# Optimization experiments

Hardware: AMD Instinct MI355X
Metric: run time of the kernel (lower is better)

The kernel has to match this reference:

```python
import jax, jax.numpy as jnp
import numpy as np

N_NODES = 100000

def setup_inputs() -> dict:
    key = jax.random.key(0)
    k1, k2, k3 = jax.random.split(key, 3)
    x = jax.random.normal(k1, (N_NODES, 64), dtype=jnp.float32)
    edge_index = jax.random.randint(k2, (2, 1600000), 0, N_NODES, dtype=jnp.int64)
    edge_weights = jax.random.uniform(k3, (1600000,), dtype=jnp.float32)
    weight = jnp.ones((1,), dtype=jnp.float32)  # MyConv.weight, reset to 1
    return {"x": x, "edge_index": edge_index, "edge_weights": edge_weights, "weight": weight}

def reference(x, edge_index, edge_weights, weight):
    src = edge_index[0]  # x_j (source nodes, messages flow source->target)
    dst = edge_index[1]  # aggregation target i
    # message: edge_weight * x_j ; aggregate: scatter-add at dst
    msgs = edge_weights[:, None] * x[src]              # [E, D]
    agg = jax.ops.segment_sum(msgs, dst, num_segments=N_NODES)  # [N, D]
    # conv1: x + weight * aggregate, then relu (Encoder only applies conv1)
    return jax.nn.relu(x + weight * agg)
```

## Files before the change

kernel.cpp:

```cpp
#include <hip/hip_runtime.h>

constexpr int N_NODES = 100000;
constexpr int D       = 64;
constexpr int N_EDGES = 1600000;
constexpr int OUT_N4  = N_NODES * D / 4;

constexpr int NPB   = 128;
constexpr int NBUCK = (N_NODES + NPB - 1) / NPB;
constexpr int BCAP  = 2560;
constexpr int CPAD  = 32;
constexpr int PTHREADS = 1024;
constexpr int EPT   = 4;
constexpr int CHUNK = PTHREADS * EPT;
constexpr int PB    = (N_EDGES + CHUNK - 1) / CHUNK;

__global__ void detect_kernel(const unsigned long long* __restrict__ ei,
                              int* __restrict__ flag) {
    if (blockIdx.x == 0 && threadIdx.x == 0) {
        int is64 = 1;
#pragma unroll
        for (int i = 0; i < 8; ++i)
            if (ei[i] >= (unsigned long long)N_NODES) is64 = 0;
        *flag = is64;
    }
}

__device__ __forceinline__ int load_idx(const void* ei_raw, int flag, long long pos) {
    if (flag) return (int)((const long long*)ei_raw)[pos];
    return ((const int*)ei_raw)[pos];
}

__device__ __forceinline__ unsigned short bf16rne(float f) {
    unsigned u = __float_as_uint(f);
    unsigned r = (u + 0x7fffu + ((u >> 16) & 1u)) >> 16;
    return (unsigned short)r;
}

__global__ void prep_kernel(const float4* __restrict__ x4,
                            ushort4* __restrict__ x16v,
                            int* __restrict__ cursor) {
    int i = blockIdx.x * blockDim.x + threadIdx.x;
    int stride = gridDim.x * blockDim.x;
    for (int j = i; j < NBUCK * CPAD; j += stride) cursor[j] = 0;
    for (; i < OUT_N4; i += stride) {
        float4 v = x4[i];
        ushort4 o;
        o.x = bf16rne(v.x); o.y = bf16rne(v.y);
        o.z = bf16rne(v.z); o.w = bf16rne(v.w);
        x16v[i] = o;
    }
}

__global__ __launch_bounds__(PTHREADS) void part_kernel(
        const void* __restrict__ ei_raw,
        const float* __restrict__ ew,
        const int* __restrict__ flag,
        int* __restrict__ cursor,
        int2* __restrict__ slots) {
    __shared__ int  hist[NBUCK];
    __shared__ int  scn[PTHREADS];
    __shared__ int  localbase[NBUCK];
    __shared__ int  runbase[NBUCK];
    __shared__ int  fill[NBUCK];
    __shared__ int2 srt[CHUNK];
    __shared__ unsigned short aux[CHUNK];

    int tid = threadIdx.x;
    for (int t = tid; t < NBUCK; t += PTHREADS) { hist[t] = 0; fill[t] = 0; }
    __syncthreads();

    int f = *flag;
    long long base = (long long)blockIdx.x * CHUNK;

    int  rb[EPT];
    int2 rrec[EPT];
#pragma unroll
    for (int it = 0; it < EPT; ++it) {
        long long e = base + it * PTHREADS + tid;
        if (e < N_EDGES) {
            int src = load_idx(ei_raw, f, e);
            int dst = load_idx(ei_raw, f, (long long)N_EDGES + e);
            int b = dst >> 7;
            rb[it] = b;
            rrec[it].x = (src << 7) | (dst & (NPB - 1));
            rrec[it].y = __float_as_int(ew[e]);
            atomicAdd(&hist[b], 1);
        } else {
            rb[it] = -1;
        }
    }
    __syncthreads();

    scn[tid] = (tid < NBUCK) ? hist[tid] : 0;
    __syncthreads();
    for (int off = 1; off < PTHREADS; off <<= 1) {
        int v = (tid >= off) ? scn[tid - off] : 0;
        __syncthreads();
        scn[tid] += v;
        __syncthreads();
    }
    if (tid < NBUCK) {
        localbase[tid] = scn[tid] - hist[tid];
        int c = hist[tid];
        runbase[tid] = (c > 0) ? atomicAdd(&cursor[tid * CPAD], c) : 0;
    }
    __syncthreads();

#pragma unroll
    for (int it = 0; it < EPT; ++it) {
        int b = rb[it];
        if (b >= 0) {
            int p = localbase[b] + atomicAdd(&fill[b], 1);
            srt[p] = rrec[it];
            aux[p] = (unsigned short)b;
        }
    }
    __syncthreads();

    int total = scn[NBUCK - 1];
    for (int i = tid; i < total; i += PTHREADS) {
        int b = aux[i];
        int g = runbase[b] + (i - localbase[b]);
        if (g < BCAP) slots[(long long)b * BCAP + g] = srt[i];
    }
}

__global__ __launch_bounds__(256) void sort_bucket_kernel(
        const int* __restrict__ cursor,
        const int2* __restrict__ slots,
        int2* __restrict__ sorted,
        int2* __restrict__ oc) {
    __shared__ int  hist[NPB];
    __shared__ int  scn[NPB];
    __shared__ int  fill[NPB];
    __shared__ int2 raw[BCAP];
    __shared__ int2 srt[BCAP];

    int tid = threadIdx.x;
    int b   = blockIdx.x;

    if (tid < NPB) { hist[tid] = 0; fill[tid] = 0; }
    __syncthreads();

    int cnt = cursor[b * CPAD];
    if (cnt > BCAP) cnt = BCAP;
    const int2* sb = slots + (long long)b * BCAP;

    for (int i = tid; i < cnt; i += 256) {
        int2 r = sb[i];
        raw[i] = r;
        atomicAdd(&hist[r.x & (NPB - 1)], 1);
    }
    __syncthreads();

    if (tid < NPB) scn[tid] = hist[tid];
    __syncthreads();
    for (int off = 1; off < NPB; off <<= 1) {
        int v = 0;
        if (tid < NPB && tid >= off) v = scn[tid - off];
        __syncthreads();
        if (tid < NPB) scn[tid] += v;
        __syncthreads();
    }

    if (tid < NPB) {
        int node = b * NPB + tid;
        if (node < N_NODES) {
            int2 v;
            v.x = b * BCAP + (scn[tid] - hist[tid]);
            v.y = hist[tid];
            oc[node] = v;
        }
    }
    __syncthreads();

    for (int i = tid; i < cnt; i += 256) {
        int2 r = raw[i];
        int dl = r.x & (NPB - 1);
        int pos = (scn[dl] - hist[dl]) + atomicAdd(&fill[dl], 1);
        srt[pos] = r;
    }
    __syncthreads();

    int2* ob = sorted + (long long)b * BCAP;
    for (int i = tid; i < cnt; i += 256) ob[i] = srt[i];
}

__global__ __launch_bounds__(256) void gather_csr_kernel(
        const unsigned short* __restrict__ x16,
        const int2* __restrict__ oc,
        const int2* __restrict__ sorted,
        const float* __restrict__ weight,
        float* __restrict__ out) {
    int lane = threadIdx.x & 63;
    int rg   = lane >> 3;
    int dg   = lane & 7;
    int node = __builtin_amdgcn_readfirstlane(
        (int)((blockIdx.x * blockDim.x + threadIdx.x) >> 6));
    if (node >= N_NODES) return;

    int2 v = oc[node];
    int beg = __builtin_amdgcn_readfirstlane(v.x);
    int cnt = __builtin_amdgcn_readfirstlane(v.y);
    const int2* s = sorted + beg;

    float acc[8];
#pragma unroll
    for (int j = 0; j < 8; ++j) acc[j] = 0.f;

    for (int k = 0; k < cnt; k += 16) {
        int iA = k + rg;
        int iB = iA + 8;
        int2 rA = s[iA < cnt ? iA : 0];
        int2 rB = s[iB < cnt ? iB : 0];
        float wA = (iA < cnt) ? __int_as_float(rA.y) : 0.f;
        float wB = (iB < cnt) ? __int_as_float(rB.y) : 0.f;
        uint4 xa = *(const uint4*)(x16 + (rA.x >> 7) * D + dg * 8);
        uint4 xb = *(const uint4*)(x16 + (rB.x >> 7) * D + dg * 8);
#pragma unroll
        for (int j = 0; j < 4; ++j) {
            unsigned ua = ((const unsigned*)&xa)[j];
            acc[2 * j]     += wA * __uint_as_float(ua << 16);
            acc[2 * j + 1] += wA * __uint_as_float(ua & 0xffff0000u);
        }
#pragma unroll
        for (int j = 0; j < 4; ++j) {
            unsigned ub = ((const unsigned*)&xb)[j];
            acc[2 * j]     += wB * __uint_as_float(ub << 16);
            acc[2 * j + 1] += wB * __uint_as_float(ub & 0xffff0000u);
        }
    }

#pragma unroll
    for (int j = 0; j < 8; ++j) {
        acc[j] += __shfl_xor(acc[j], 8, 64);
        acc[j] += __shfl_xor(acc[j], 16, 64);
        acc[j] += __shfl_xor(acc[j], 32, 64);
    }

    if (rg == 0) {
        float W = weight[0];
        uint4 xs = *(const uint4*)(x16 + node * D + dg * 8);
        float o[8];
#pragma unroll
        for (int j = 0; j < 4; ++j) {
            unsigned us = ((const unsigned*)&xs)[j];
            o[2 * j]     = fmaxf(__uint_as_float(us << 16)         + W * acc[2 * j],     0.f);
            o[2 * j + 1] = fmaxf(__uint_as_float(us & 0xffff0000u) + W * acc[2 * j + 1], 0.f);
        }
        float4* po = (float4*)(out + node * D + dg * 8);
        po[0] = make_float4(o[0], o[1], o[2], o[3]);
        po[1] = make_float4(o[4], o[5], o[6], o[7]);
    }
}

__global__ void init_out_kernel(const float4* __restrict__ x4,
                                float4* __restrict__ out4) {
    int i = blockIdx.x * blockDim.x + threadIdx.x;
    int stride = gridDim.x * blockDim.x;
    for (; i < OUT_N4; i += stride) out4[i] = x4[i];
}

__global__ __launch_bounds__(256) void scatter_atomic_kernel(
        const float* __restrict__ x,
        const void* __restrict__ ei_raw,
        const float* __restrict__ ew,
        const float* __restrict__ weight,
        const int* __restrict__ flag,
        float* __restrict__ out) {
    long long gid = (long long)blockIdx.x * blockDim.x + threadIdx.x;
    int e = (int)(gid >> 6);
    int d = (int)(gid & 63);
    if (e >= N_EDGES) return;
    int f = *flag;
    int src = load_idx(ei_raw, f, e);
    int dst = load_idx(ei_raw, f, (long long)N_EDGES + e);
    float w = weight[0] * ew[e];
    atomicAdd(&out[dst * D + d], w * x[src * D + d]);
}

__global__ void relu_kernel(float4* __restrict__ out4) {
    int i = blockIdx.x * blockDim.x + threadIdx.x;
    int stride = gridDim.x * blockDim.x;
    for (; i < OUT_N4; i += stride) {
        float4 v = out4[i];
        v.x = fmaxf(v.x, 0.0f);
        v.y = fmaxf(v.y, 0.0f);
        v.z = fmaxf(v.z, 0.0f);
        v.w = fmaxf(v.w, 0.0f);
        out4[i] = v;
    }
}

extern "C" void kernel_launch(void* const* d_in, const int* in_sizes, int n_in,
                              void* d_out, int out_size, void* d_ws, size_t ws_size,
                              hipStream_t stream) {
    const float* x      = (const float*)d_in[0];
    const void*  ei     = d_in[1];
    const float* ew     = (const float*)d_in[2];
    const float* weight = (const float*)d_in[3];
    float* out = (float*)d_out;

    char* w = (char*)d_ws;
    auto align256 = [](size_t v) { return (v + 255) & ~(size_t)255; };

    size_t off = 0;
    int* flag = (int*)(w + off);        off = align256(off + 4);
    int* cursor = (int*)(w + off);      off = align256(off + (size_t)NBUCK * CPAD * 4);
    int2* oc = (int2*)(w + off);        off = align256(off + (size_t)N_NODES * 8);
    unsigned short* x16 = (unsigned short*)(w + off);
                                        off = align256(off + (size_t)N_NODES * D * 2);
    int2* slots = (int2*)(w + off);     off = align256(off + (size_t)NBUCK * BCAP * 8);
    int2* sorted = (int2*)(w + off);    off = align256(off + (size_t)NBUCK * BCAP * 8);
    size_t needed = off;

    detect_kernel<<<1, 64, 0, stream>>>((const unsigned long long*)ei, flag);

    if (ws_size >= needed) {
        prep_kernel<<<2048, 256, 0, stream>>>((const float4*)x, (ushort4*)x16, cursor);
        part_kernel<<<PB, PTHREADS, 0, stream>>>(ei, ew, flag, cursor, slots);
        sort_bucket_kernel<<<NBUCK, 256, 0, stream>>>(cursor, slots, sorted, oc);
        gather_csr_kernel<<<(N_NODES * 64 + 255) / 256, 256, 0, stream>>>(
            x16, oc, sorted, weight, out);
    } else {
        init_out_kernel<<<2048, 256, 0, stream>>>((const float4*)x, (float4*)out);
        long long total = (long long)N_EDGES * 64;
        scatter_atomic_kernel<<<(int)((total + 255) / 256), 256, 0, stream>>>(
            x, ei, ew, weight, flag, out);
        relu_kernel<<<2048, 256, 0, stream>>>((float4*)out);
    }
}
```

Measured before the change: 94.22 us.

## Fuse bucket sort with CSR gather and use wave-shuffle scans

The per-bucket sort and the gather are merged into one kernel. Each 1024-thread block sorts its bucket's edges in shared memory and then gathers neighbour features straight from that sorted LDS copy, so the sorted array and the offset/count array no longer pass through global memory and one launch is removed. The block-wide LDS prefix scans in both partition and sort are replaced with wavefront shuffle scans, which cuts the number of barriers. In exchange, gather parallelism drops to 782 blocks of 16 waves, each wave handling 8 nodes in sequence. The large LDS footprint (about 40KB) also limits occupancy.

```diff
diff --git a/kernel.cpp b/kernel.cpp
--- a/kernel.cpp
+++ b/kernel.cpp
@@ -58,14 +58,17 @@
         int* __restrict__ cursor,
         int2* __restrict__ slots) {
     __shared__ int  hist[NBUCK];
-    __shared__ int  scn[PTHREADS];
     __shared__ int  localbase[NBUCK];
     __shared__ int  runbase[NBUCK];
     __shared__ int  fill[NBUCK];
+    __shared__ int  wsum[16];
+    __shared__ int  tot;
     __shared__ int2 srt[CHUNK];
     __shared__ unsigned short aux[CHUNK];
 
-    int tid = threadIdx.x;
+    int tid  = threadIdx.x;
+    int wv   = tid >> 6;
+    int lane = tid & 63;
     for (int t = tid; t < NBUCK; t += PTHREADS) { hist[t] = 0; fill[t] = 0; }
     __syncthreads();
 
@@ -91,16 +94,29 @@
     }
     __syncthreads();
 
-    scn[tid] = (tid < NBUCK) ? hist[tid] : 0;
-    __syncthreads();
-    for (int off = 1; off < PTHREADS; off <<= 1) {
-        int v = (tid >= off) ? scn[tid - off] : 0;
-        __syncthreads();
-        scn[tid] += v;
-        __syncthreads();
-    }
+    int h = (tid < NBUCK) ? hist[tid] : 0;
+    int v = h;
+#pragma unroll
+    for (int off = 1; off < 64; off <<= 1) {
+        int u = __shfl_up(v, off, 64);
+        if (lane >= off) v += u;
+    }
+    if (lane == 63) wsum[wv] = v;
+    __syncthreads();
+    if (wv == 0 && lane < 16) {
+        int s = wsum[lane];
+        int t2 = s;
+#pragma unroll
+        for (int off = 1; off < 16; off <<= 1) {
+            int u = __shfl_up(t2, off, 64);
+            if (lane >= off) t2 += u;
+        }
+        wsum[lane] = t2 - s;
+        if (lane == 15) tot = t2;
+    }
+    __syncthreads();
     if (tid < NBUCK) {
-        localbase[tid] = scn[tid] - hist[tid];
+        localbase[tid] = (v - h) + wsum[wv];
         int c = hist[tid];
         runbase[tid] = (c > 0) ? atomicAdd(&cursor[tid * CPAD], c) : 0;
     }
@@ -117,7 +133,7 @@
     }
     __syncthreads();
 
-    int total = scn[NBUCK - 1];
+    int total = tot;
     for (int i = tid; i < total; i += PTHREADS) {
         int b = aux[i];
         int g = runbase[b] + (i - localbase[b]);
@@ -125,19 +141,22 @@
     }
 }
 
-__global__ __launch_bounds__(256) void sort_bucket_kernel(
+__global__ __launch_bounds__(PTHREADS) void sg_kernel(
+        const unsigned short* __restrict__ x16,
         const int* __restrict__ cursor,
         const int2* __restrict__ slots,
-        int2* __restrict__ sorted,
-        int2* __restrict__ oc) {
+        const float* __restrict__ weight,
+        float* __restrict__ out) {
     __shared__ int  hist[NPB];
-    __shared__ int  scn[NPB];
+    __shared__ int  nbeg[NPB];
     __shared__ int  fill[NPB];
     __shared__ int2 raw[BCAP];
     __shared__ int2 srt[BCAP];
 
-    int tid = threadIdx.x;
-    int b   = blockIdx.x;
+    int tid  = threadIdx.x;
+    int wv   = tid >> 6;
+    int lane = tid & 63;
+    int b    = blockIdx.x;
 
     if (tid < NPB) { hist[tid] = 0; fill[tid] = 0; }
     __syncthreads();
@@ -146,111 +165,94 @@
     if (cnt > BCAP) cnt = BCAP;
     const int2* sb = slots + (long long)b * BCAP;
 
-    for (int i = tid; i < cnt; i += 256) {
+    for (int i = tid; i < cnt; i += PTHREADS) {
         int2 r = sb[i];
         raw[i] = r;
         atomicAdd(&hist[r.x & (NPB - 1)], 1);
     }
     __syncthreads();
 
-    if (tid < NPB) scn[tid] = hist[tid];
-    __syncthreads();
-    for (int off = 1; off < NPB; off <<= 1) {
-        int v = 0;
-        if (tid < NPB && tid >= off) v = scn[tid - off];
-        __syncthreads();
-        if (tid < NPB) scn[tid] += v;
-        __syncthreads();
-    }
-
-    if (tid < NPB) {
-        int node = b * NPB + tid;
-        if (node < N_NODES) {
-            int2 v;
-            v.x = b * BCAP + (scn[tid] - hist[tid]);
-            v.y = hist[tid];
-            oc[node] = v;
-        }
-    }
-    __syncthreads();
-
-    for (int i = tid; i < cnt; i += 256) {
+    if (wv == 0) {
+        int h0 = hist[2 * lane];
+        int h1 = hist[2 * lane + 1];
+        int s  = h0 + h1;
+        int v  = s;
+#pragma unroll
+        for (int off = 1; off < 64; off <<= 1) {
+            int u = __shfl_up(v, off, 64);
+            if (lane >= off) v += u;
+        }
+        int excl = v - s;
+        nbeg[2 * lane]     = excl;
+        nbeg[2 * lane + 1] = excl + h0;
+    }
+    __syncthreads();
+
+    for (int i = tid; i < cnt; i += PTHREADS) {
         int2 r = raw[i];
         int dl = r.x & (NPB - 1);
-        int pos = (scn[dl] - hist[dl]) + atomicAdd(&fill[dl], 1);
+        int pos = nbeg[dl] + atomicAdd(&fill[dl], 1);
         srt[pos] = r;
     }
     __syncthreads();
 
-    int2* ob = sorted + (long long)b * BCAP;
-    for (int i = tid; i < cnt; i += 256) ob[i] = srt[i];
-}
-
-__global__ __launch_bounds__(256) void gather_csr_kernel(
-        const unsigned short* __restrict__ x16,
-        const int2* __restrict__ oc,
-        const int2* __restrict__ sorted,
-        const float* __restrict__ weight,
-        float* __restrict__ out) {
-    int lane = threadIdx.x & 63;
-    int rg   = lane >> 3;
-    int dg   = lane & 7;
-    int node = __builtin_amdgcn_readfirstlane(
-        (int)((blockIdx.x * blockDim.x + threadIdx.x) >> 6));
-    if (node >= N_NODES) return;
-
-    int2 v = oc[node];
-    int beg = __builtin_amdgcn_readfirstlane(v.x);
-    int cnt = __builtin_amdgcn_readfirstlane(v.y);
-    const int2* s = sorted + beg;
-
-    float acc[8];
-#pragma unroll
-    for (int j = 0; j < 8; ++j) acc[j] = 0.f;
-
-    for (int k = 0; k < cnt; k += 16) {
-        int iA = k + rg;
-        int iB = iA + 8;
-        int2 rA = s[iA < cnt ? iA : 0];
-        int2 rB = s[iB < cnt ? iB : 0];
-        float wA = (iA < cnt) ? __int_as_float(rA.y) : 0.f;
-        float wB = (iB < cnt) ? __int_as_float(rB.y) : 0.f;
-        uint4 xa = *(const uint4*)(x16 + (rA.x >> 7) * D + dg * 8);
-        uint4 xb = *(const uint4*)(x16 + (rB.x >> 7) * D + dg * 8);
-#pragma unroll
-        for (int j = 0; j < 4; ++j) {
-            unsigned ua = ((const unsigned*)&xa)[j];
-            acc[2 * j]     += wA * __uint_as_float(ua << 16);
-            acc[2 * j + 1] += wA * __uint_as_float(ua & 0xffff0000u);
-        }
-#pragma unroll
-        for (int j = 0; j < 4; ++j) {
-            unsigned ub = ((const unsigned*)&xb)[j];
-            acc[2 * j]     += wB * __uint_as_float(ub << 16);
-            acc[2 * j + 1] += wB * __uint_as_float(ub & 0xffff0000u);
-        }
-    }
-
-#pragma unroll
-    for (int j = 0; j < 8; ++j) {
-        acc[j] += __shfl_xor(acc[j], 8, 64);
-        acc[j] += __shfl_xor(acc[j], 16, 64);
-        acc[j] += __shfl_xor(acc[j], 32, 64);
-    }
-
-    if (rg == 0) {
-        float W = weight[0];
-        uint4 xs = *(const uint4*)(x16 + node * D + dg * 8);
-        float o[8];
-#pragma unroll
-        for (int j = 0; j < 4; ++j) {
-            unsigned us = ((const unsigned*)&xs)[j];
-            o[2 * j]     = fmaxf(__uint_as_float(us << 16)         + W * acc[2 * j],     0.f);
-            o[2 * j + 1] = fmaxf(__uint_as_float(us & 0xffff0000u) + W * acc[2 * j + 1], 0.f);
-        }
-        float4* po = (float4*)(out + node * D + dg * 8);
-        po[0] = make_float4(o[0], o[1], o[2], o[3]);
-        po[1] = make_float4(o[4], o[5], o[6], o[7]);
+    int rg = lane >> 3;
+    int dg = lane & 7;
+    float W = weight[0];
+
+    for (int dl = wv * 8; dl < wv * 8 + 8; ++dl) {
+        int node = b * NPB + dl;
+        if (node >= N_NODES) continue;
+        int nb = nbeg[dl];
+        int nc = hist[dl];
+
+        float acc[8];
+#pragma unroll
+        for (int j = 0; j < 8; ++j) acc[j] = 0.f;
+
+        for (int k = 0; k < nc; k += 16) {
+            int iA = k + rg;
+            int iB = iA + 8;
+            int2 rA = srt[nb + (iA < nc ? iA : 0)];
+            int2 rB = srt[nb + (iB < nc ? iB : 0)];
+            float wA = (iA < nc) ? __int_as_float(rA.y) : 0.f;
+            float wB = (iB < nc) ? __int_as_float(rB.y) : 0.f;
+            uint4 xa = *(const uint4*)(x16 + (rA.x >> 7) * D + dg * 8);
+            uint4 xb = *(const uint4*)(x16 + (rB.x >> 7) * D + dg * 8);
+#pragma unroll
+            for (int j = 0; j < 4; ++j) {
+                unsigned ua = ((const unsigned*)&xa)[j];
+                acc[2 * j]     += wA * __uint_as_float(ua << 16);
+                acc[2 * j + 1] += wA * __uint_as_float(ua & 0xffff0000u);
+            }
+#pragma unroll
+            for (int j = 0; j < 4; ++j) {
+                unsigned ub = ((const unsigned*)&xb)[j];
+                acc[2 * j]     += wB * __uint_as_float(ub << 16);
+                acc[2 * j + 1] += wB * __uint_as_float(ub & 0xffff0000u);
+            }
+        }
+
+#pragma unroll
+        for (int j = 0; j < 8; ++j) {
+            acc[j] += __shfl_xor(acc[j], 8, 64);
+            acc[j] += __shfl_xor(acc[j], 16, 64);
+            acc[j] += __shfl_xor(acc[j], 32, 64);
+        }
+
+        if (rg == 0) {
+            uint4 xs = *(const uint4*)(x16 + node * D + dg * 8);
+            float o[8];
+#pragma unroll
+            for (int j = 0; j < 4; ++j) {
+                unsigned us = ((const unsigned*)&xs)[j];
+                o[2 * j]     = fmaxf(__uint_as_float(us << 16)         + W * acc[2 * j],     0.f);
+                o[2 * j + 1] = fmaxf(__uint_as_float(us & 0xffff0000u) + W * acc[2 * j + 1], 0.f);
+            }
+            float4* po = (float4*)(out + node * D + dg * 8);
+            po[0] = make_float4(o[0], o[1], o[2], o[3]);
+            po[1] = make_float4(o[4], o[5], o[6], o[7]);
+        }
     }
 }
 
@@ -307,11 +309,9 @@
     size_t off = 0;
     int* flag = (int*)(w + off);        off = align256(off + 4);
     int* cursor = (int*)(w + off);      off = align256(off + (size_t)NBUCK * CPAD * 4);
-    int2* oc = (int2*)(w + off);        off = align256(off + (size_t)N_NODES * 8);
     unsigned short* x16 = (unsigned short*)(w + off);
                                         off = align256(off + (size_t)N_NODES * D * 2);
     int2* slots = (int2*)(w + off);     off = align256(off + (size_t)NBUCK * BCAP * 8);
-    int2* sorted = (int2*)(w + off);    off = align256(off + (size_t)NBUCK * BCAP * 8);
     size_t needed = off;
 
     detect_kernel<<<1, 64, 0, stream>>>((const unsigned long long*)ei, flag);
@@ -319,9 +319,7 @@
     if (ws_size >= needed) {
         prep_kernel<<<2048, 256, 0, stream>>>((const float4*)x, (ushort4*)x16, cursor);
         part_kernel<<<PB, PTHREADS, 0, stream>>>(ei, ew, flag, cursor, slots);
-        sort_bucket_kernel<<<NBUCK, 256, 0, stream>>>(cursor, slots, sorted, oc);
-        gather_csr_kernel<<<(N_NODES * 64 + 255) / 256, 256, 0, stream>>>(
-            x16, oc, sorted, weight, out);
+        sg_kernel<<<NBUCK, PTHREADS, 0, stream>>>(x16, cursor, slots, weight, out);
     } else {
         init_out_kernel<<<2048, 256, 0, stream>>>((const float4*)x, (float4*)out);
         long long total = (long long)N_EDGES * 64;
```

Measured after the change: 89.13 us. -5.4%, faster.
